# Optimization experiments

Hardware: AMD Instinct MI355X
Metric: run time of the kernel (lower is better)

The kernel has to match this reference:

```python
import jax, jax.numpy as jnp
import numpy as np

NUM_NODES = 256
INPUTS = list(range(8))
OUTPUTS = list(range(248, 256))
V_MEAS = np.array(sorted(set(range(NUM_NODES)) - set(OUTPUTS)))  # 0..247
V_CORR = np.array(sorted(set(range(NUM_NODES)) - set(INPUTS)))   # 8..255
INNER_LR = 0.1
INNER_ITER = 200
B1, B2, ADAM_EPS = 0.9, 0.999, 1e-8
CAUSAL_EPS = 0.1


def _parity_loss(G, A_sub):
    # G, A_sub: [B, m, c]; enforces sum(A*G) odd
    S = jnp.sum(A_sub * G, axis=2)                 # [B, m]
    val = jnp.sin(jnp.pi * S / 2) ** 2
    return jnp.mean((val - 1.0) ** 2)


def _causal_loss(G, T):
    # T: [B, n]; penalty = relu(T_u - T_v + eps)
    T_u = T[:, V_MEAS][:, :, None]                 # [B, m, 1]
    T_v = T[:, V_CORR][:, None, :]                 # [B, 1, c]
    penalty = jax.nn.relu(T_u - T_v + CAUSAL_EPS)  # [B, m, c]
    return jnp.mean(G * penalty)


def setup_inputs() -> dict:
    key = jax.random.key(0)
    k1, k2, k3 = jax.random.split(key, 3)
    B = 128
    adj_batch = jax.random.uniform(k1, (B, NUM_NODES, NUM_NODES), dtype=jnp.float32)
    G_logits0 = jax.random.normal(k2, (B, len(V_MEAS), len(V_CORR)), dtype=jnp.float32)
    T0 = jax.random.uniform(k3, (B, NUM_NODES), dtype=jnp.float32)
    return {"adj_batch": adj_batch, "G_logits0": G_logits0, "T0": T0}


def reference(adj_batch, G_logits0, T0):
    A_sub = adj_batch[:, V_MEAS][:, :, V_CORR]     # [B, m, c]
    A_det = jax.lax.stop_gradient(A_sub)           # adj is detached in the inner loop

    def inner_loss(params):
        G_logits, T = params
        G = jax.nn.sigmoid(G_logits)
        loss_p = _parity_loss(G, A_det)
        loss_c = _causal_loss(G, T)
        loss_s = jnp.mean(jnp.abs(G - 0.5)) * 0.1
        return loss_p + loss_c + loss_s

    grad_fn = jax.grad(inner_loss)

    def adam_step(carry, t):
        params, m, v = carry
        g = grad_fn(params)
        m = jax.tree.map(lambda m_, g_: B1 * m_ + (1 - B1) * g_, m, g)
        v = jax.tree.map(lambda v_, g_: B2 * v_ + (1 - B2) * g_ * g_, v, g)
        bc1 = 1.0 - B1 ** t
        bc2 = 1.0 - B2 ** t
        params = jax.tree.map(
            lambda p, m_, v_: p - INNER_LR * (m_ / bc1) / (jnp.sqrt(v_ / bc2) + ADAM_EPS),
            params, m, v)
        return (params, m, v), None

    params0 = (G_logits0, T0)
    zeros = jax.tree.map(jnp.zeros_like, params0)
    steps = jnp.arange(1, INNER_ITER + 1, dtype=jnp.float32)
    (params, _, _), _ = jax.lax.scan(adam_step, (params0, zeros, zeros), steps)

    G_logits, T = jax.lax.stop_gradient(params)    # .detach() in torch source
    G_final = jax.nn.sigmoid(G_logits)
    final_parity = _parity_loss(G_final, A_sub)    # differentiable w.r.t. adj_batch
    final_causal = _causal_loss(G_final, T)
    return (final_parity + final_causal, final_parity, final_causal)
```

## Files before the change

### kernel.cpp

```cpp
#include <hip/hip_runtime.h>
#include <hip/hip_cooperative_groups.h>
#include <math.h>

namespace cg = cooperative_groups;

#define B_N   128
#define M_N   248
#define C_N   248
#define NODES 256
#define NT    (B_N*NODES)
#define NG    (B_N*M_N*C_N)

#define GRID  256
#define TPB   512
#define HROWS 124
#define KMAX  16
#define DYN_LDS (KMAX*TPB*16)

#define PI_F     3.14159265358979323846f
#define INV_BM   (1.0f/31744.0f)
#define INV_BMC  (1.0f/7872512.0f)

__device__ __forceinline__ float rcp_nr(float x) {
    float r = __builtin_amdgcn_rcpf(x);
    return r * fmaf(-x, r, 2.0f);
}
__device__ __forceinline__ float sigm_fast(float x) {
    return rcp_nr(1.0f + __expf(-x));
}
__device__ __forceinline__ float sigm(float x) {
    float z = expf(-fabsf(x));
    return (x >= 0.0f) ? 1.0f/(1.0f+z) : z/(1.0f+z);
}
__device__ __forceinline__ float sgn(float x) {
    return (x > 0.0f) ? 1.0f : ((x < 0.0f) ? -1.0f : 0.0f);
}

extern __shared__ float4 vG_lds[];

__global__ __launch_bounds__(TPB) __attribute__((amdgpu_waves_per_eu(2, 2)))
void persist_kernel(
    const float* __restrict__ adj, const float* __restrict__ Gl0,
    const float* __restrict__ T0,
    float* __restrict__ gTu,
    float* __restrict__ gTv,
    float* __restrict__ accum,
    float* __restrict__ out)
{
    __shared__ float T_lds[NODES], mT_lds[NODES], vT_lds[NODES];
    __shared__ float red[16];

    cg::grid_group grid = cg::this_grid();
    const int tid  = threadIdx.x;
    const int blkI = blockIdx.x;
    const int b    = ((blkI >> 4) << 3) | (blkI & 7);
    const int h    = (blkI >> 3) & 1;
    const int wave = tid >> 6, lane = tid & 63;
    const bool v62 = (lane < 62);
    const int jb   = v62 ? 4*lane : 0;

    if (tid < NODES) {
        T_lds[tid]  = T0[b*NODES + tid];
        mT_lds[tid] = 0.0f;
        vT_lds[tid] = 0.0f;
    }
    #pragma unroll
    for (int k = 0; k < KMAX; ++k)
        vG_lds[k*TPB + tid] = float4{0.0f, 0.0f, 0.0f, 0.0f};

    float Glr[KMAX][4], mGr[KMAX][4];
    #pragma unroll
    for (int k = 0; k < KMAX; ++k) {
        #pragma unroll
        for (int s = 0; s < 4; ++s) { Glr[k][s] = 0.0f; mGr[k][s] = 0.0f; }
        const int lr = wave + 8*k;
        if (lr < HROWS && v62) {
            const int i = h*HROWS + lr;
            const float4 g4 = *(const float4*)&Gl0[((size_t)(b*M_N + i))*C_N + jb];
            Glr[k][0] = g4.x; Glr[k][1] = g4.y; Glr[k][2] = g4.z; Glr[k][3] = g4.w;
        }
    }
    __syncthreads();

    double pw1d = 1.0, pw2d = 1.0;
    #pragma unroll 1
    for (int t = 1; t <= 200; ++t) {
        const float bc1p = (float)(1.0 - pw1d), bc2p = (float)(1.0 - pw2d);
        pw1d *= 0.9; pw2d *= 0.999;
        const float bc1 = (float)(1.0 - pw1d), bc2 = (float)(1.0 - pw2d);
        const float ibc1 = 1.0f/bc1, ibc2 = 1.0f/bc2;
        const int pw = t & 1, ps = (t-1) & 1;

        if (t > 1) {
            grid.sync();
            if (tid < NODES) {
                float g = 0.0f;
                if (tid < M_N) g += gTu[ps*(B_N*M_N) + b*M_N + tid];
                if (tid >= 8) {
                    const float* gp = gTv + (size_t)ps*(B_N*16*256)
                                    + (size_t)(b*16)*256 + (tid-8);
                    float s = 0.0f;
                    #pragma unroll
                    for (int p = 0; p < 16; ++p) s += gp[p*256];
                    g -= s;
                }
                g *= INV_BMC;
                float m_ = 0.9f*mT_lds[tid] + 0.1f*g;
                float v_ = 0.999f*vT_lds[tid] + 0.001f*(g*g);
                mT_lds[tid] = m_; vT_lds[tid] = v_;
                T_lds[tid] = T_lds[tid] - 0.1f*(m_/bc1p)/(sqrtf(v_/bc2p) + 1e-8f);
            }
            __syncthreads();
        }

        const float Tv0 = T_lds[jb+8],  Tv1 = T_lds[jb+9];
        const float Tv2 = T_lds[jb+10], Tv3 = T_lds[jb+11];

        float av0 = 0.0f, av1 = 0.0f, av2 = 0.0f, av3 = 0.0f;
        #pragma unroll
        for (int k = 0; k < KMAX; ++k) {
            const int lr = wave + 8*k;
            if (lr < HROWS) {
                const int i = h*HROWS + lr;
                float4 a4 = {0.0f, 0.0f, 0.0f, 0.0f};
                if (v62)
                    a4 = *(const float4*)&adj[((size_t)(b*NODES + i))*NODES + 8 + jb];

                const float G0 = sigm_fast(Glr[k][0]), G1 = sigm_fast(Glr[k][1]);
                const float G2 = sigm_fast(Glr[k][2]), G3 = sigm_fast(Glr[k][3]);

                const float Tu = T_lds[i];
                const float d0 = v62 ? (Tu - Tv0 + 0.1f) : 0.0f;
                const float d1 = v62 ? (Tu - Tv1 + 0.1f) : 0.0f;
                const float d2 = v62 ? (Tu - Tv2 + 0.1f) : 0.0f;
                const float d3 = v62 ? (Tu - Tv3 + 0.1f) : 0.0f;
                const float p0 = fmaxf(d0,0.0f), p1 = fmaxf(d1,0.0f);
                const float p2 = fmaxf(d2,0.0f), p3 = fmaxf(d3,0.0f);
                const float mk0 = (d0>0.0f)?1.0f:0.0f;
                const float mk1 = (d1>0.0f)?1.0f:0.0f;
                const float mk2 = (d2>0.0f)?1.0f:0.0f;
                const float mk3 = (d3>0.0f)?1.0f:0.0f;

                float sp = a4.x*G0 + a4.y*G1 + a4.z*G2 + a4.w*G3;
                float gu = G0*mk0 + G1*mk1 + G2*mk2 + G3*mk3;
                #pragma unroll
                for (int off = 32; off > 0; off >>= 1) {
                    sp += __shfl_xor(sp, off, 64);
                    gu += __shfl_xor(gu, off, 64);
                }
                av0 += G0*mk0; av1 += G1*mk1; av2 += G2*mk2; av3 += G3*mk3;

                const float half_arg = (PI_F*sp)*0.5f;
                const float sv = __sinf(half_arg), cv = __cosf(half_arg);
                const float coefP = 2.0f*(sv*sv-1.0f)*sv*cv*PI_F*INV_BM;

                if (lane == 0) gTu[pw*(B_N*M_N) + b*M_N + i] = gu;

                float4 vv = vG_lds[k*TPB + tid];
                #define DO_SLOT(Gx, ax, px, vx, s_) do {                             \
                    float dG  = coefP*(ax) + (px)*INV_BMC + 0.1f*INV_BMC*sgn((Gx)-0.5f); \
                    float grd = dG * (Gx) * (1.0f - (Gx));                           \
                    float m_ = 0.9f*mGr[k][s_] + 0.1f*grd;                           \
                    float v_ = 0.999f*(vx) + 0.001f*(grd*grd);                       \
                    mGr[k][s_] = m_; (vx) = v_;                                      \
                    Glr[k][s_] -= 0.1f*(m_*ibc1)*rcp_nr(sqrtf(v_*ibc2) + 1e-8f);     \
                } while (0)
                DO_SLOT(G0, a4.x, p0, vv.x, 0);
                DO_SLOT(G1, a4.y, p1, vv.y, 1);
                DO_SLOT(G2, a4.z, p2, vv.z, 2);
                DO_SLOT(G3, a4.w, p3, vv.w, 3);
                #undef DO_SLOT
                vG_lds[k*TPB + tid] = vv;
            }
        }
        {
            float* gpw = gTv + (size_t)pw*(B_N*16*256) + (size_t)(b*16 + h*8 + wave)*256;
            ((float4*)gpw)[lane] = float4{av0, av1, av2, av3};
        }
    }

    grid.sync();
    if (tid < NODES) {
        const float bc1p = (float)(1.0 - pw1d), bc2p = (float)(1.0 - pw2d);
        float g = 0.0f;
        if (tid < M_N) g += gTu[0*(B_N*M_N) + b*M_N + tid];
        if (tid >= 8) {
            const float* gp = gTv + (size_t)(b*16)*256 + (tid-8);
            float s = 0.0f;
            #pragma unroll
            for (int p = 0; p < 16; ++p) s += gp[p*256];
            g -= s;
        }
        g *= INV_BMC;
        float m_ = 0.9f*mT_lds[tid] + 0.1f*g;
        float v_ = 0.999f*vT_lds[tid] + 0.001f*(g*g);
        T_lds[tid] = T_lds[tid] - 0.1f*(m_/bc1p)/(sqrtf(v_/bc2p) + 1e-8f);
    }
    __syncthreads();

    {
        const float Tv0 = T_lds[jb+8],  Tv1 = T_lds[jb+9];
        const float Tv2 = T_lds[jb+10], Tv3 = T_lds[jb+11];
        float pacc = 0.0f, cacc = 0.0f;
        #pragma unroll
        for (int k = 0; k < KMAX; ++k) {
            const int lr = wave + 8*k;
            if (lr < HROWS) {
                const int i = h*HROWS + lr;
                float4 a4 = {0.0f, 0.0f, 0.0f, 0.0f};
                if (v62)
                    a4 = *(const float4*)&adj[((size_t)(b*NODES + i))*NODES + 8 + jb];
                const float G0 = sigm_fast(Glr[k][0]), G1 = sigm_fast(Glr[k][1]);
                const float G2 = sigm_fast(Glr[k][2]), G3 = sigm_fast(Glr[k][3]);
                const float Tu = T_lds[i];
                const float p0 = v62 ? fmaxf(Tu - Tv0 + 0.1f, 0.0f) : 0.0f;
                const float p1 = v62 ? fmaxf(Tu - Tv1 + 0.1f, 0.0f) : 0.0f;
                const float p2 = v62 ? fmaxf(Tu - Tv2 + 0.1f, 0.0f) : 0.0f;
                const float p3 = v62 ? fmaxf(Tu - Tv3 + 0.1f, 0.0f) : 0.0f;

                float sp = a4.x*G0 + a4.y*G1 + a4.z*G2 + a4.w*G3;
                float cp = G0*p0 + G1*p1 + G2*p2 + G3*p3;
                #pragma unroll
                for (int off = 32; off > 0; off >>= 1) {
                    sp += __shfl_xor(sp, off, 64);
                    cp += __shfl_xor(cp, off, 64);
                }
                if (lane == 0) {
                    const float sv = sinf((PI_F*sp)*0.5f);
                    const float dd = sv*sv - 1.0f;
                    pacc += dd*dd;
                    cacc += cp;
                }
            }
        }
        if (lane == 0) { red[wave] = pacc; red[8+wave] = cacc; }
    }
    __syncthreads();
    if (tid == 0) {
        float rp = 0.0f, rc = 0.0f;
        #pragma unroll
        for (int w = 0; w < 8; ++w) { rp += red[w]; rc += red[8+w]; }
        atomicAdd(&accum[0], rp);
        atomicAdd(&accum[1], rc);
    }
    __threadfence();
    grid.sync();
    if (blkI == 0 && tid == 0) {
        const float p = __hip_atomic_load(&accum[0], __ATOMIC_RELAXED, __HIP_MEMORY_SCOPE_AGENT) * INV_BM;
        const float c = __hip_atomic_load(&accum[1], __ATOMIC_RELAXED, __HIP_MEMORY_SCOPE_AGENT) * INV_BMC;
        out[0] = p + c;
        out[1] = p;
        out[2] = c;
    }
}

#define NBLK  8
#define RPB   31

__global__ __launch_bounds__(256) void iter_kernel(
    const float* __restrict__ adj, float* __restrict__ Gl,
    float* __restrict__ mG, float* __restrict__ vG,
    float* __restrict__ T_state, float* __restrict__ mT, float* __restrict__ vT,
    float* __restrict__ gTu, float* __restrict__ gTv,
    int t, float bc1p, float bc2p, float bc1, float bc2)
{
    __shared__ float T_lds[NODES];
    __shared__ float gv_lds[4*NODES];
    const int tid = threadIdx.x;
    const int b   = blockIdx.x >> 3;
    const int blk = blockIdx.x & 7;

    if (t == 1) {
        T_lds[tid] = T_state[b*NODES + tid];
    } else {
        const int rs = t & 1, ws2 = (t+1) & 1, ps = (t-1) & 1;
        const int idx = b*NODES + tid;
        float Tval = T_state[rs*NT + idx];
        float g = 0.0f;
        if (tid < M_N) g += gTu[ps*(B_N*M_N) + b*M_N + tid];
        if (tid >= 8) {
            const float* gp = gTv + (size_t)ps*(B_N*NBLK*C_N) + (size_t)b*NBLK*C_N + (tid-8);
            float s = 0.0f;
            #pragma unroll
            for (int k = 0; k < NBLK; ++k) s += gp[k*C_N];
            g -= s;
        }
        g *= INV_BMC;
        float m_ = 0.9f*mT[rs*NT+idx] + 0.1f*g;
        float v_ = 0.999f*vT[rs*NT+idx] + 0.001f*(g*g);
        float newT = Tval - 0.1f*(m_/bc1p)/(sqrtf(v_/bc2p) + 1e-8f);
        T_state[ws2*NT+idx] = newT;
        mT[ws2*NT+idx] = m_;
        vT[ws2*NT+idx] = v_;
        T_lds[tid] = newT;
    }
    gv_lds[tid] = 0.0f; gv_lds[256+tid] = 0.0f; gv_lds[512+tid] = 0.0f; gv_lds[768+tid] = 0.0f;
    __syncthreads();

    const int wave = tid >> 6, lane = tid & 63;
    const int pw = t & 1;
    const int j0 = lane, j1 = lane+64, j2 = lane+128, j3 = lane+192;
    const bool v3 = (lane < 56);
    float av0 = 0.0f, av1 = 0.0f, av2 = 0.0f, av3 = 0.0f;

    for (int r = wave; r < RPB; r += 4) {
        const int i = blk*RPB + r;
        const size_t arow = ((size_t)(b*NODES + i))*NODES + 8;
        const size_t grow = ((size_t)(b*M_N + i))*C_N;

        float gl0 = Gl[grow+j0], gl1 = Gl[grow+j1], gl2 = Gl[grow+j2];
        float gl3 = v3 ? Gl[grow+j3] : 0.0f;
        float a0 = adj[arow+j0], a1 = adj[arow+j1], a2 = adj[arow+j2];
        float a3 = v3 ? adj[arow+j3] : 0.0f;
        float G0 = sigm(gl0), G1 = sigm(gl1), G2 = sigm(gl2), G3 = sigm(gl3);

        float Tu = T_lds[i];
        float d0 = Tu - T_lds[j0+8] + 0.1f;
        float d1 = Tu - T_lds[j1+8] + 0.1f;
        float d2 = Tu - T_lds[j2+8] + 0.1f;
        float d3 = v3 ? (Tu - T_lds[j3+8] + 0.1f) : 0.0f;
        float p0 = fmaxf(d0, 0.0f), p1 = fmaxf(d1, 0.0f);
        float p2 = fmaxf(d2, 0.0f), p3 = fmaxf(d3, 0.0f);
        float mk0 = (d0 > 0.0f) ? 1.0f : 0.0f;
        float mk1 = (d1 > 0.0f) ? 1.0f : 0.0f;
        float mk2 = (d2 > 0.0f) ? 1.0f : 0.0f;
        float mk3 = (v3 && d3 > 0.0f) ? 1.0f : 0.0f;

        float sp = a0*G0 + a1*G1 + a2*G2 + (v3 ? a3*G3 : 0.0f);
        float gu = G0*mk0 + G1*mk1 + G2*mk2 + G3*mk3;
        #pragma unroll
        for (int off = 32; off > 0; off >>= 1) {
            sp += __shfl_xor(sp, off, 64);
            gu += __shfl_xor(gu, off, 64);
        }
        av0 += G0*mk0; av1 += G1*mk1; av2 += G2*mk2; av3 += G3*mk3;

        float half_arg = (PI_F*sp)*0.5f;
        float sv = sinf(half_arg), cv = cosf(half_arg);
        float val = sv*sv;
        float coefP = 2.0f*(val-1.0f)*sv*cv*PI_F*INV_BM;

        if (lane == 0) gTu[pw*(B_N*M_N) + b*M_N + i] = gu;

        #define DO_SLOT(Gx, glx, ax, px, jx, valid) do { if (valid) {            \
            float dG  = coefP*(ax) + (px)*INV_BMC + 0.1f*INV_BMC*sgn((Gx)-0.5f); \
            float grd = dG * (Gx) * (1.0f - (Gx));                               \
            float m_ = 0.9f*mG[grow+(jx)] + 0.1f*grd;                            \
            float v_ = 0.999f*vG[grow+(jx)] + 0.001f*(grd*grd);                  \
            mG[grow+(jx)] = m_; vG[grow+(jx)] = v_;                              \
            Gl[grow+(jx)] = (glx) - 0.1f*(m_/bc1)/(sqrtf(v_/bc2)+1e-8f);         \
        } } while (0)
        DO_SLOT(G0, gl0, a0, p0, j0, true);
        DO_SLOT(G1, gl1, a1, p1, j1, true);
        DO_SLOT(G2, gl2, a2, p2, j2, true);
        DO_SLOT(G3, gl3, a3, p3, j3, v3);
        #undef DO_SLOT
    }

    gv_lds[wave*256 + j0] = av0;
    gv_lds[wave*256 + j1] = av1;
    gv_lds[wave*256 + j2] = av2;
    if (v3) gv_lds[wave*256 + j3] = av3;
    __syncthreads();
    if (tid < C_N) {
        float s = gv_lds[tid] + gv_lds[256+tid] + gv_lds[512+tid] + gv_lds[768+tid];
        gTv[(size_t)pw*(B_N*NBLK*C_N) + (size_t)(b*NBLK + blk)*C_N + tid] = s;
    }
}

__global__ __launch_bounds__(256) void t_fin_kernel(
    float* __restrict__ T_state, const float* __restrict__ mT, const float* __restrict__ vT,
    const float* __restrict__ gTu, const float* __restrict__ gTv,
    float bc1p, float bc2p)
{
    const int b = blockIdx.x, tid = threadIdx.x;
    const int idx = b*NODES + tid;
    float Tval = T_state[1*NT + idx];
    float g = 0.0f;
    if (tid < M_N) g += gTu[0*(B_N*M_N) + b*M_N + tid];
    if (tid >= 8) {
        const float* gp = gTv + (size_t)b*NBLK*C_N + (tid-8);
        float s = 0.0f;
        #pragma unroll
        for (int k = 0; k < NBLK; ++k) s += gp[k*C_N];
        g -= s;
    }
    g *= INV_BMC;
    float m_ = 0.9f*mT[1*NT+idx] + 0.1f*g;
    float v_ = 0.999f*vT[1*NT+idx] + 0.001f*(g*g);
    T_state[0*NT+idx] = Tval - 0.1f*(m_/bc1p)/(sqrtf(v_/bc2p) + 1e-8f);
}

__global__ __launch_bounds__(256) void loss_kernel(
    const float* __restrict__ adj, const float* __restrict__ Gl,
    const float* __restrict__ T_state, float* __restrict__ accum)
{
    __shared__ float T_lds[NODES];
    __shared__ float red[8];
    const int tid = threadIdx.x;
    const int b = blockIdx.x >> 3, blk = blockIdx.x & 7;
    T_lds[tid] = T_state[b*NODES + tid];
    __syncthreads();
    const int wave = tid >> 6, lane = tid & 63;
    const int j0 = lane, j1 = lane+64, j2 = lane+128, j3 = lane+192;
    const bool v3 = (lane < 56);
    float pacc = 0.0f, cacc = 0.0f;

    for (int r = wave; r < RPB; r += 4) {
        const int i = blk*RPB + r;
        const size_t arow = ((size_t)(b*NODES + i))*NODES + 8;
        const size_t grow = ((size_t)(b*M_N + i))*C_N;
        float gl0 = Gl[grow+j0], gl1 = Gl[grow+j1], gl2 = Gl[grow+j2];
        float gl3 = v3 ? Gl[grow+j3] : 0.0f;
        float a0 = adj[arow+j0], a1 = adj[arow+j1], a2 = adj[arow+j2];
        float a3 = v3 ? adj[arow+j3] : 0.0f;
        float G0 = sigm(gl0), G1 = sigm(gl1), G2 = sigm(gl2), G3 = sigm(gl3);

        float Tu = T_lds[i];
        float p0 = fmaxf(Tu - T_lds[j0+8] + 0.1f, 0.0f);
        float p1 = fmaxf(Tu - T_lds[j1+8] + 0.1f, 0.0f);
        float p2 = fmaxf(Tu - T_lds[j2+8] + 0.1f, 0.0f);
        float p3 = v3 ? fmaxf(Tu - T_lds[j3+8] + 0.1f, 0.0f) : 0.0f;

        float sp = a0*G0 + a1*G1 + a2*G2 + (v3 ? a3*G3 : 0.0f);
        float cp = G0*p0 + G1*p1 + G2*p2 + (v3 ? G3*p3 : 0.0f);
        #pragma unroll
        for (int off = 32; off > 0; off >>= 1) {
            sp += __shfl_xor(sp, off, 64);
            cp += __shfl_xor(cp, off, 64);
        }
        if (lane == 0) {
            float sv = sinf((PI_F*sp)*0.5f);
            float dd = sv*sv - 1.0f;
            pacc += dd*dd;
            cacc += cp;
        }
    }
    if (lane == 0) { red[wave] = pacc; red[4+wave] = cacc; }
    __syncthreads();
    if (tid == 0) {
        atomicAdd(&accum[0], red[0]+red[1]+red[2]+red[3]);
        atomicAdd(&accum[1], red[4]+red[5]+red[6]+red[7]);
    }
}

__global__ void finish_kernel(const float* __restrict__ accum, float* __restrict__ out) {
    if (threadIdx.x == 0 && blockIdx.x == 0) {
        float p = accum[0] / 31744.0f;
        float c = accum[1] / 7872512.0f;
        out[0] = p + c;
        out[1] = p;
        out[2] = c;
    }
}

extern "C" void kernel_launch(void* const* d_in, const int* in_sizes, int n_in,
                              void* d_out, int out_size, void* d_ws, size_t ws_size,
                              hipStream_t stream) {
    const float* adj = (const float*)d_in[0];
    float* Gl        = (float*)d_in[1];
    const float* T0  = (const float*)d_in[2];
    float* out       = (float*)d_out;
    float* ws        = (float*)d_ws;

    int dev = 0;  hipGetDevice(&dev);
    int numCU = 0;
    hipDeviceGetAttribute(&numCU, hipDeviceAttributeMultiprocessorCount, dev);
    hipError_t aerr = hipFuncSetAttribute((const void*)persist_kernel,
                                          hipFuncAttributeMaxDynamicSharedMemorySize,
                                          DYN_LDS);
    int maxB = 0;
    hipError_t oerr = hipOccupancyMaxActiveBlocksPerMultiprocessor(
                          &maxB, persist_kernel, TPB, DYN_LDS);
    const bool coop_ok = (aerr == hipSuccess) && (oerr == hipSuccess) &&
                         (maxB >= 1) && ((long)maxB * (long)numCU >= GRID);

    if (coop_ok) {
        float* gTu   = ws;
        float* gTv   = gTu + 2*B_N*M_N;
        float* accum = gTv + (size_t)2*B_N*16*256;
        hipMemsetAsync(accum, 0, 2*sizeof(float), stream);

        const float* Gl0 = Gl;
        void* args[] = { (void*)&adj, (void*)&Gl0, (void*)&T0,
                         (void*)&gTu, (void*)&gTv, (void*)&accum, (void*)&out };
        hipLaunchCooperativeKernel((void*)persist_kernel,
                                   dim3(GRID), dim3(TPB), args, DYN_LDS, stream);
    } else {
        float* mG      = ws;
        float* vG      = mG + NG;
        float* T_state = vG + NG;
        float* mT      = T_state + 2*NT;
        float* vT      = mT + 2*NT;
        float* gTu     = vT + 2*NT;
        float* gTv     = gTu + 2*B_N*M_N;
        float* accum   = gTv + (size_t)2*B_N*NBLK*C_N;

        hipMemsetAsync(mG, 0, (size_t)2*NG*sizeof(float), stream);
        hipMemsetAsync(mT, 0, (size_t)4*NT*sizeof(float), stream);
        hipMemsetAsync(accum, 0, 2*sizeof(float), stream);
        hipMemcpyAsync(T_state, T0, NT*sizeof(float), hipMemcpyDeviceToDevice, stream);

        for (int t = 1; t <= 200; ++t) {
            float bc1p = 1.0f - (float)pow(0.9,   (double)(t-1));
            float bc2p = 1.0f - (float)pow(0.999, (double)(t-1));
            float bc1  = 1.0f - (float)pow(0.9,   (double)t);
            float bc2  = 1.0f - (float)pow(0.999, (double)t);
            iter_kernel<<<dim3(B_N*NBLK), dim3(256), 0, stream>>>(
                adj, Gl, mG, vG, T_state, mT, vT, gTu, gTv, t, bc1p, bc2p, bc1, bc2);
        }
        {
            float bc1p = 1.0f - (float)pow(0.9,   200.0);
            float bc2p = 1.0f - (float)pow(0.999, 200.0);
            t_fin_kernel<<<dim3(B_N), dim3(256), 0, stream>>>(T_state, mT, vT, gTu, gTv, bc1p, bc2p);
        }
        loss_kernel<<<dim3(B_N*NBLK), dim3(256), 0, stream>>>(adj, Gl, T_state, accum);
        finish_kernel<<<1, 64, 0, stream>>>(accum, out);
    }
}
```

Measured before the change: 8.243 ms.

## Double persistent block width to 16 waves and halve rows per wave

Raises the cooperative persistent kernel from 512 to 1024 threads per block, so each wave owns 8 rows instead of 16. Register state moves from arrays to named float4 variables, and the per-block gTv partial slices double from 16 to 32 to match. The aim is more waves per CU to hide the adj load latency and the transcendental work in each of the 200 Adam steps. In exchange, the T update after each grid sync sums twice as many slices, the per-thread register budget shrinks, and the waves_per_eu hint is removed.

```diff
diff --git a/kernel.cpp b/kernel.cpp
--- a/kernel.cpp
+++ b/kernel.cpp
@@ -12,9 +12,11 @@
 #define NG    (B_N*M_N*C_N)
 
 #define GRID  256
-#define TPB   512
+#define TPB   1024
+#define WAVES 16
 #define HROWS 124
-#define KMAX  16
+#define KMAX  8
+#define SLICES 32
 #define DYN_LDS (KMAX*TPB*16)
 
 #define PI_F     3.14159265358979323846f
@@ -38,7 +40,7 @@
 
 extern __shared__ float4 vG_lds[];
 
-__global__ __launch_bounds__(TPB) __attribute__((amdgpu_waves_per_eu(2, 2)))
+__global__ __launch_bounds__(TPB)
 void persist_kernel(
     const float* __restrict__ adj, const float* __restrict__ Gl0,
     const float* __restrict__ T0,
@@ -48,7 +50,7 @@
     float* __restrict__ out)
 {
     __shared__ float T_lds[NODES], mT_lds[NODES], vT_lds[NODES];
-    __shared__ float red[16];
+    __shared__ float red[2*WAVES];
 
     cg::grid_group grid = cg::this_grid();
     const int tid  = threadIdx.x;
@@ -58,6 +60,10 @@
     const int wave = tid >> 6, lane = tid & 63;
     const bool v62 = (lane < 62);
     const int jb   = v62 ? 4*lane : 0;
+    const int iBase = h*HROWS + wave;
+    const float* adjRow0 = adj + ((size_t)(b*NODES + iBase))*NODES + 8 + jb;
+
+    #define ROW_OK(k) ((k) < 7 || wave < 12)
 
     if (tid < NODES) {
         T_lds[tid]  = T0[b*NODES + tid];
@@ -68,18 +74,16 @@
     for (int k = 0; k < KMAX; ++k)
         vG_lds[k*TPB + tid] = float4{0.0f, 0.0f, 0.0f, 0.0f};
 
-    float Glr[KMAX][4], mGr[KMAX][4];
-    #pragma unroll
-    for (int k = 0; k < KMAX; ++k) {
-        #pragma unroll
-        for (int s = 0; s < 4; ++s) { Glr[k][s] = 0.0f; mGr[k][s] = 0.0f; }
-        const int lr = wave + 8*k;
-        if (lr < HROWS && v62) {
-            const int i = h*HROWS + lr;
-            const float4 g4 = *(const float4*)&Gl0[((size_t)(b*M_N + i))*C_N + jb];
-            Glr[k][0] = g4.x; Glr[k][1] = g4.y; Glr[k][2] = g4.z; Glr[k][3] = g4.w;
-        }
-    }
+    float4 gl0, gl1, gl2, gl3, gl4, gl5, gl6, gl7;
+    float4 mm0, mm1, mm2, mm3, mm4, mm5, mm6, mm7;
+    #define LOADG(k, glv, mmv) do {                                               \
+        glv = float4{0.0f,0.0f,0.0f,0.0f}; mmv = float4{0.0f,0.0f,0.0f,0.0f};     \
+        if (ROW_OK(k) && v62)                                                     \
+            glv = *(const float4*)&Gl0[((size_t)(b*M_N + iBase + 16*(k)))*C_N + jb]; \
+    } while (0)
+    LOADG(0, gl0, mm0); LOADG(1, gl1, mm1); LOADG(2, gl2, mm2); LOADG(3, gl3, mm3);
+    LOADG(4, gl4, mm4); LOADG(5, gl5, mm5); LOADG(6, gl6, mm6); LOADG(7, gl7, mm7);
+    #undef LOADG
     __syncthreads();
 
     double pw1d = 1.0, pw2d = 1.0;
@@ -97,11 +101,11 @@
                 float g = 0.0f;
                 if (tid < M_N) g += gTu[ps*(B_N*M_N) + b*M_N + tid];
                 if (tid >= 8) {
-                    const float* gp = gTv + (size_t)ps*(B_N*16*256)
-                                    + (size_t)(b*16)*256 + (tid-8);
+                    const float* gp = gTv + (size_t)ps*(B_N*SLICES*256)
+                                    + (size_t)(b*SLICES)*256 + (tid-8);
                     float s = 0.0f;
                     #pragma unroll
-                    for (int p = 0; p < 16; ++p) s += gp[p*256];
+                    for (int p = 0; p < SLICES; ++p) s += gp[p*256];
                     g -= s;
                 }
                 g *= INV_BMC;
@@ -115,66 +119,63 @@
 
         const float Tv0 = T_lds[jb+8],  Tv1 = T_lds[jb+9];
         const float Tv2 = T_lds[jb+10], Tv3 = T_lds[jb+11];
-
         float av0 = 0.0f, av1 = 0.0f, av2 = 0.0f, av3 = 0.0f;
-        #pragma unroll
-        for (int k = 0; k < KMAX; ++k) {
-            const int lr = wave + 8*k;
-            if (lr < HROWS) {
-                const int i = h*HROWS + lr;
-                float4 a4 = {0.0f, 0.0f, 0.0f, 0.0f};
-                if (v62)
-                    a4 = *(const float4*)&adj[((size_t)(b*NODES + i))*NODES + 8 + jb];
-
-                const float G0 = sigm_fast(Glr[k][0]), G1 = sigm_fast(Glr[k][1]);
-                const float G2 = sigm_fast(Glr[k][2]), G3 = sigm_fast(Glr[k][3]);
-
-                const float Tu = T_lds[i];
-                const float d0 = v62 ? (Tu - Tv0 + 0.1f) : 0.0f;
-                const float d1 = v62 ? (Tu - Tv1 + 0.1f) : 0.0f;
-                const float d2 = v62 ? (Tu - Tv2 + 0.1f) : 0.0f;
-                const float d3 = v62 ? (Tu - Tv3 + 0.1f) : 0.0f;
-                const float p0 = fmaxf(d0,0.0f), p1 = fmaxf(d1,0.0f);
-                const float p2 = fmaxf(d2,0.0f), p3 = fmaxf(d3,0.0f);
-                const float mk0 = (d0>0.0f)?1.0f:0.0f;
-                const float mk1 = (d1>0.0f)?1.0f:0.0f;
-                const float mk2 = (d2>0.0f)?1.0f:0.0f;
-                const float mk3 = (d3>0.0f)?1.0f:0.0f;
-
-                float sp = a4.x*G0 + a4.y*G1 + a4.z*G2 + a4.w*G3;
-                float gu = G0*mk0 + G1*mk1 + G2*mk2 + G3*mk3;
-                #pragma unroll
-                for (int off = 32; off > 0; off >>= 1) {
-                    sp += __shfl_xor(sp, off, 64);
-                    gu += __shfl_xor(gu, off, 64);
-                }
-                av0 += G0*mk0; av1 += G1*mk1; av2 += G2*mk2; av3 += G3*mk3;
-
-                const float half_arg = (PI_F*sp)*0.5f;
-                const float sv = __sinf(half_arg), cv = __cosf(half_arg);
-                const float coefP = 2.0f*(sv*sv-1.0f)*sv*cv*PI_F*INV_BM;
-
-                if (lane == 0) gTu[pw*(B_N*M_N) + b*M_N + i] = gu;
-
-                float4 vv = vG_lds[k*TPB + tid];
-                #define DO_SLOT(Gx, ax, px, vx, s_) do {                             \
-                    float dG  = coefP*(ax) + (px)*INV_BMC + 0.1f*INV_BMC*sgn((Gx)-0.5f); \
-                    float grd = dG * (Gx) * (1.0f - (Gx));                           \
-                    float m_ = 0.9f*mGr[k][s_] + 0.1f*grd;                           \
-                    float v_ = 0.999f*(vx) + 0.001f*(grd*grd);                       \
-                    mGr[k][s_] = m_; (vx) = v_;                                      \
-                    Glr[k][s_] -= 0.1f*(m_*ibc1)*rcp_nr(sqrtf(v_*ibc2) + 1e-8f);     \
-                } while (0)
-                DO_SLOT(G0, a4.x, p0, vv.x, 0);
-                DO_SLOT(G1, a4.y, p1, vv.y, 1);
-                DO_SLOT(G2, a4.z, p2, vv.z, 2);
-                DO_SLOT(G3, a4.w, p3, vv.w, 3);
-                #undef DO_SLOT
-                vG_lds[k*TPB + tid] = vv;
-            }
-        }
+
+        #define DO_SLOT(Gx, ax, px, mx, vx) do {                                     \
+            float dG  = coefP*(ax) + (px)*INV_BMC + 0.1f*INV_BMC*sgn((Gx)-0.5f);     \
+            float grd = dG * (Gx) * (1.0f - (Gx));                                   \
+            float m_ = 0.9f*(mx) + 0.1f*grd;                                         \
+            float v_ = 0.999f*(vx) + 0.001f*(grd*grd);                               \
+            (mx) = m_; (vx) = v_;                                                    \
+            glslot -= 0.1f*(m_*ibc1)*rcp_nr(sqrtf(v_*ibc2) + 1e-8f);                 \
+        } while (0)
+
+        #define ROW_STEP(k, glv, mmv) do { if (ROW_OK(k)) {                          \
+            const int i = iBase + 16*(k);                                            \
+            float4 a4 = float4{0.0f,0.0f,0.0f,0.0f};                                 \
+            if (v62) a4 = *(const float4*)(adjRow0 + (size_t)(16*(k))*NODES);        \
+            const float G0 = sigm_fast(glv.x), G1 = sigm_fast(glv.y);                \
+            const float G2 = sigm_fast(glv.z), G3 = sigm_fast(glv.w);                \
+            const float Tu = T_lds[i];                                               \
+            float d0, d1, d2, d3;                                                    \
+            if (v62) { d0 = Tu-Tv0+0.1f; d1 = Tu-Tv1+0.1f;                           \
+                       d2 = Tu-Tv2+0.1f; d3 = Tu-Tv3+0.1f; }                         \
+            else     { d0 = d1 = d2 = d3 = 0.0f; }                                   \
+            const float p0 = fmaxf(d0,0.0f), p1 = fmaxf(d1,0.0f);                    \
+            const float p2 = fmaxf(d2,0.0f), p3 = fmaxf(d3,0.0f);                    \
+            const float mk0 = (d0>0.0f)?1.0f:0.0f, mk1 = (d1>0.0f)?1.0f:0.0f;        \
+            const float mk2 = (d2>0.0f)?1.0f:0.0f, mk3 = (d3>0.0f)?1.0f:0.0f;        \
+            float sp = a4.x*G0 + a4.y*G1 + a4.z*G2 + a4.w*G3;                        \
+            float gu = G0*mk0 + G1*mk1 + G2*mk2 + G3*mk3;                            \
+            sp += __shfl_xor(sp,32,64); gu += __shfl_xor(gu,32,64);                  \
+            sp += __shfl_xor(sp,16,64); gu += __shfl_xor(gu,16,64);                  \
+            sp += __shfl_xor(sp, 8,64); gu += __shfl_xor(gu, 8,64);                  \
+            sp += __shfl_xor(sp, 4,64); gu += __shfl_xor(gu, 4,64);                  \
+            sp += __shfl_xor(sp, 2,64); gu += __shfl_xor(gu, 2,64);                  \
+            sp += __shfl_xor(sp, 1,64); gu += __shfl_xor(gu, 1,64);                  \
+            av0 += G0*mk0; av1 += G1*mk1; av2 += G2*mk2; av3 += G3*mk3;              \
+            const float half_arg = (PI_F*sp)*0.5f;                                   \
+            const float sv = __sinf(half_arg), cv = __cosf(half_arg);                \
+            const float coefP = 2.0f*(sv*sv-1.0f)*sv*cv*PI_F*INV_BM;                 \
+            if (lane == 0) gTu[pw*(B_N*M_N) + b*M_N + i] = gu;                       \
+            float4 vv = vG_lds[(k)*TPB + tid];                                       \
+            { float& glslot = glv.x; DO_SLOT(G0, a4.x, p0, mmv.x, vv.x); }           \
+            { float& glslot = glv.y; DO_SLOT(G1, a4.y, p1, mmv.y, vv.y); }           \
+            { float& glslot = glv.z; DO_SLOT(G2, a4.z, p2, mmv.z, vv.z); }           \
+            { float& glslot = glv.w; DO_SLOT(G3, a4.w, p3, mmv.w, vv.w); }           \
+            vG_lds[(k)*TPB + tid] = vv;                                              \
+        } } while (0)
+
+        ROW_STEP(0, gl0, mm0); ROW_STEP(1, gl1, mm1);
+        ROW_STEP(2, gl2, mm2); ROW_STEP(3, gl3, mm3);
+        ROW_STEP(4, gl4, mm4); ROW_STEP(5, gl5, mm5);
+        ROW_STEP(6, gl6, mm6); ROW_STEP(7, gl7, mm7);
+        #undef ROW_STEP
+        #undef DO_SLOT
+
         {
-            float* gpw = gTv + (size_t)pw*(B_N*16*256) + (size_t)(b*16 + h*8 + wave)*256;
+            float* gpw = gTv + (size_t)pw*(B_N*SLICES*256)
+                       + (size_t)(b*SLICES + h*WAVES + wave)*256;
             ((float4*)gpw)[lane] = float4{av0, av1, av2, av3};
         }
     }
@@ -185,10 +186,10 @@
         float g = 0.0f;
         if (tid < M_N) g += gTu[0*(B_N*M_N) + b*M_N + tid];
         if (tid >= 8) {
-            const float* gp = gTv + (size_t)(b*16)*256 + (tid-8);
+            const float* gp = gTv + (size_t)(b*SLICES)*256 + (tid-8);
             float s = 0.0f;
             #pragma unroll
-            for (int p = 0; p < 16; ++p) s += gp[p*256];
+            for (int p = 0; p < SLICES; ++p) s += gp[p*256];
             g -= s;
         }
         g *= INV_BMC;
@@ -202,44 +203,45 @@
         const float Tv0 = T_lds[jb+8],  Tv1 = T_lds[jb+9];
         const float Tv2 = T_lds[jb+10], Tv3 = T_lds[jb+11];
         float pacc = 0.0f, cacc = 0.0f;
-        #pragma unroll
-        for (int k = 0; k < KMAX; ++k) {
-            const int lr = wave + 8*k;
-            if (lr < HROWS) {
-                const int i = h*HROWS + lr;
-                float4 a4 = {0.0f, 0.0f, 0.0f, 0.0f};
-                if (v62)
-                    a4 = *(const float4*)&adj[((size_t)(b*NODES + i))*NODES + 8 + jb];
-                const float G0 = sigm_fast(Glr[k][0]), G1 = sigm_fast(Glr[k][1]);
-                const float G2 = sigm_fast(Glr[k][2]), G3 = sigm_fast(Glr[k][3]);
-                const float Tu = T_lds[i];
-                const float p0 = v62 ? fmaxf(Tu - Tv0 + 0.1f, 0.0f) : 0.0f;
-                const float p1 = v62 ? fmaxf(Tu - Tv1 + 0.1f, 0.0f) : 0.0f;
-                const float p2 = v62 ? fmaxf(Tu - Tv2 + 0.1f, 0.0f) : 0.0f;
-                const float p3 = v62 ? fmaxf(Tu - Tv3 + 0.1f, 0.0f) : 0.0f;
-
-                float sp = a4.x*G0 + a4.y*G1 + a4.z*G2 + a4.w*G3;
-                float cp = G0*p0 + G1*p1 + G2*p2 + G3*p3;
-                #pragma unroll
-                for (int off = 32; off > 0; off >>= 1) {
-                    sp += __shfl_xor(sp, off, 64);
-                    cp += __shfl_xor(cp, off, 64);
-                }
-                if (lane == 0) {
-                    const float sv = sinf((PI_F*sp)*0.5f);
-                    const float dd = sv*sv - 1.0f;
-                    pacc += dd*dd;
-                    cacc += cp;
-                }
-            }
-        }
-        if (lane == 0) { red[wave] = pacc; red[8+wave] = cacc; }
+
+        #define ROW_LOSS(k, glv) do { if (ROW_OK(k)) {                               \
+            const int i = iBase + 16*(k);                                            \
+            float4 a4 = float4{0.0f,0.0f,0.0f,0.0f};                                 \
+            if (v62) a4 = *(const float4*)(adjRow0 + (size_t)(16*(k))*NODES);        \
+            const float G0 = sigm_fast(glv.x), G1 = sigm_fast(glv.y);                \
+            const float G2 = sigm_fast(glv.z), G3 = sigm_fast(glv.w);                \
+            const float Tu = T_lds[i];                                               \
+            const float p0 = v62 ? fmaxf(Tu-Tv0+0.1f, 0.0f) : 0.0f;                  \
+            const float p1 = v62 ? fmaxf(Tu-Tv1+0.1f, 0.0f) : 0.0f;                  \
+            const float p2 = v62 ? fmaxf(Tu-Tv2+0.1f, 0.0f) : 0.0f;                  \
+            const float p3 = v62 ? fmaxf(Tu-Tv3+0.1f, 0.0f) : 0.0f;                  \
+            float sp = a4.x*G0 + a4.y*G1 + a4.z*G2 + a4.w*G3;                        \
+            float cp = G0*p0 + G1*p1 + G2*p2 + G3*p3;                                \
+            sp += __shfl_xor(sp,32,64); cp += __shfl_xor(cp,32,64);                  \
+            sp += __shfl_xor(sp,16,64); cp += __shfl_xor(cp,16,64);                  \
+            sp += __shfl_xor(sp, 8,64); cp += __shfl_xor(cp, 8,64);                  \
+            sp += __shfl_xor(sp, 4,64); cp += __shfl_xor(cp, 4,64);                  \
+            sp += __shfl_xor(sp, 2,64); cp += __shfl_xor(cp, 2,64);                  \
+            sp += __shfl_xor(sp, 1,64); cp += __shfl_xor(cp, 1,64);                  \
+            if (lane == 0) {                                                         \
+                const float sv = sinf((PI_F*sp)*0.5f);                               \
+                const float dd = sv*sv - 1.0f;                                       \
+                pacc += dd*dd;                                                       \
+                cacc += cp;                                                          \
+            }                                                                        \
+        } } while (0)
+
+        ROW_LOSS(0, gl0); ROW_LOSS(1, gl1); ROW_LOSS(2, gl2); ROW_LOSS(3, gl3);
+        ROW_LOSS(4, gl4); ROW_LOSS(5, gl5); ROW_LOSS(6, gl6); ROW_LOSS(7, gl7);
+        #undef ROW_LOSS
+
+        if (lane == 0) { red[wave] = pacc; red[WAVES+wave] = cacc; }
     }
     __syncthreads();
     if (tid == 0) {
         float rp = 0.0f, rc = 0.0f;
         #pragma unroll
-        for (int w = 0; w < 8; ++w) { rp += red[w]; rc += red[8+w]; }
+        for (int w = 0; w < WAVES; ++w) { rp += red[w]; rc += red[WAVES+w]; }
         atomicAdd(&accum[0], rp);
         atomicAdd(&accum[1], rc);
     }
@@ -252,6 +254,7 @@
         out[1] = p;
         out[2] = c;
     }
+    #undef ROW_OK
 }
 
 #define NBLK  8
@@ -478,7 +481,7 @@
     if (coop_ok) {
         float* gTu   = ws;
         float* gTv   = gTu + 2*B_N*M_N;
-        float* accum = gTv + (size_t)2*B_N*16*256;
+        float* accum = gTv + (size_t)2*B_N*SLICES*256;
         hipMemsetAsync(accum, 0, 2*sizeof(float), stream);
 
         const float* Gl0 = Gl;
```

After: 8.151 ms. About the same (-1.1%).
